# Optimization experiments

Measured on AMD Instinct MI355X. Metric: run time of the kernel, lower is better.

Reference implementation:

```python
import jax, jax.numpy as jnp
import numpy as np
from jax import lax

DT = 0.01
INPUT_SCALER = 20.0
BETA1 = 1.0


def setup_inputs() -> dict:
    key = jax.random.key(0)
    k1, k2, k3 = jax.random.split(key, 3)
    bs, T, d, nk = 8, 64, 32, 32
    X_r = jax.random.normal(k1, (bs, T, d, d, nk), dtype=jnp.float32)
    X_i = jax.random.normal(k2, (bs, T, d, d, nk), dtype=jnp.float32)
    # omegas ~ U(min_omega, max_omega) * 2*pi (Gaussian blur omitted: it only
    # smooths the fixed parameter initialization, not the forward math)
    min_omega, max_omega = 0.1, 1.0
    omegas = (jax.random.uniform(k3, (d, d, nk), dtype=jnp.float32)
              * (max_omega - min_omega) + min_omega) * (2 * 3.1415)
    return {"X_r": X_r, "X_i": X_i, "omegas": omegas}


def reference(X_r, X_i, omegas):
    bs, T, d1, d2, nk = X_r.shape
    # time-major for scan: [T, bs, d, d, nk]
    Xr_t = jnp.moveaxis(X_r, 1, 0)
    Xi_t = jnp.moveaxis(X_i, 1, 0)

    r0 = jnp.ones((bs, d1, d2, nk), dtype=X_r.dtype)
    phi0 = jnp.zeros((bs, d1, d2, nk), dtype=X_r.dtype)

    def step(carry, xs):
        r, phi = carry
        xr, xi = xs
        input_r = INPUT_SCALER * xr * jnp.cos(phi)
        input_phi = INPUT_SCALER * xi * jnp.sin(phi)
        r = r + ((1.0 - BETA1 * r * r) * r + input_r) * DT
        phi = phi + (omegas - input_phi) * DT
        return (r, phi), (r, phi)

    _, (r_arr, phi_arr) = lax.scan(step, (r0, phi0), (Xr_t, Xi_t))
    # back to batch-major: [bs, T, d, d, nk]
    r_arr = jnp.moveaxis(r_arr, 0, 1)
    phi_arr = jnp.moveaxis(phi_arr, 0, 1)
    return r_arr * jnp.cos(phi_arr), r_arr * jnp.sin(phi_arr)
```

## Files before the change

### kernel.cpp

```cpp
#include <hip/hip_runtime.h>


#define T_STEPS 64
#define CHV2    16384
#define BS      8
#define DEPTH   16

typedef float v2f __attribute__((ext_vector_type(2)));

__global__ __launch_bounds__(256)
void hopf_scan_kernel(const float* __restrict__ Xr,
                      const float* __restrict__ Xi,
                      const float* __restrict__ Om,
                      float* __restrict__ out)
{
    const float DT = 0.01f;
    const float SC = 20.0f;
    const float S1 = -1.6666667e-1f, S2 = 8.3333333e-3f,
                S3 = -1.9841270e-4f, S4 = 2.7557319e-6f;
    const float C1 = -0.5f, C2 = 4.1666667e-2f,
                C3 = -1.3888889e-3f, C4 = 2.4801587e-5f;

    const v2f* __restrict__ vXr = (const v2f*)Xr;
    const v2f* __restrict__ vXi = (const v2f*)Xi;
    const v2f* __restrict__ vOm = (const v2f*)Om;
    v2f* __restrict__ vout      = (v2f*)out;

    int tid = blockIdx.x * blockDim.x + threadIdx.x;
    int b   = tid >> 14;
    int cv  = tid & (CHV2 - 1);

    v2f om = vOm[cv];

    const size_t stride = CHV2;
    size_t base = (size_t)(b * T_STEPS) * stride + cv;
    const v2f* pxr = vXr + base;
    const v2f* pxi = vXi + base;
    v2f* po0 = vout + base;
    v2f* po1 = po0 + (size_t)BS * T_STEPS * stride;

    float r[2]  = {1.f, 1.f};
    float co[2] = {1.f, 1.f};
    float si[2] = {0.f, 0.f};

    v2f xr[DEPTH], xi[DEPTH];
    #pragma unroll
    for (int i = 0; i < DEPTH; ++i) {
        xr[i] = __builtin_nontemporal_load(pxr + (size_t)i * stride);
        xi[i] = __builtin_nontemporal_load(pxi + (size_t)i * stride);
    }

    #pragma unroll
    for (int t = 0; t < T_STEPS; ++t) {
        const int s = t & (DEPTH - 1);
        v2f axr = xr[s];
        v2f axi = xi[s];
        if (t + DEPTH < T_STEPS) {
            xr[s] = __builtin_nontemporal_load(pxr + (size_t)(t + DEPTH) * stride);
            xi[s] = __builtin_nontemporal_load(pxi + (size_t)(t + DEPTH) * stride);
        }

        v2f o0, o1;
        #pragma unroll
        for (int j = 0; j < 2; ++j) {
            float ir   = SC * axr[j] * co[j];
            float dphi = (om[j] - SC * axi[j] * si[j]) * DT;
            r[j] = r[j] + ((1.f - r[j] * r[j]) * r[j] + ir) * DT;

            float u  = dphi * dphi;
            float sp = fmaf(u, S4, S3);
            sp = fmaf(u, sp, S2);
            sp = fmaf(u, sp, S1);
            sp = fmaf(u, sp, 1.f);
            sp *= dphi;
            float cp = fmaf(u, C4, C3);
            cp = fmaf(u, cp, C2);
            cp = fmaf(u, cp, C1);
            cp = fmaf(u, cp, 1.f);

            float nco = fmaf(co[j], cp, -si[j] * sp);
            float nsi = fmaf(si[j], cp,  co[j] * sp);
            co[j] = nco; si[j] = nsi;

            o0[j] = r[j] * co[j];
            o1[j] = r[j] * si[j];
        }

        size_t off = (size_t)t * stride;
        po0[off] = o0;
        po1[off] = o1;
    }
}

extern "C" void kernel_launch(void* const* d_in, const int* in_sizes, int n_in,
                              void* d_out, int out_size, void* d_ws, size_t ws_size,
                              hipStream_t stream) {
    const float* Xr = (const float*)d_in[0];
    const float* Xi = (const float*)d_in[1];
    const float* Om = (const float*)d_in[2];
    float* out = (float*)d_out;

    dim3 block(256);
    dim3 grid(BS * CHV2 / 256);
    hopf_scan_kernel<<<grid, block, 0, stream>>>(Xr, Xi, Om, out);
}
```

Baseline: 225.7 us.

## Warp-specialize producer waves loading inputs into LDS ring via global_load_lds

Splits each 512-thread block into four producer waves that stream Xr/Xi time slices directly into a 4-slot LDS ring buffer with global_load_lds, and four consumer waves that read from LDS and run the recurrence. The two groups coordinate with barriers and explicit vmcnt waits. This replaces the per-thread register prefetch of 16 timesteps and is meant to cut register pressure and keep more loads in flight. The cost is barrier synchronization on every two timesteps, half of each block's waves doing no compute, and fragile hand-tuned waitcnt logic.

```diff
diff --git a/kernel.cpp b/kernel.cpp
--- a/kernel.cpp
+++ b/kernel.cpp
@@ -1,94 +1,138 @@
 #include <hip/hip_runtime.h>
+#include <stdint.h>
 
 
 #define T_STEPS 64
 #define CHV2    16384
 #define BS      8
-#define DEPTH   16
+#define CPB     256
+#define SLOTB   4096
 
 typedef float v2f __attribute__((ext_vector_type(2)));
+typedef __attribute__((address_space(3))) uint32_t as3_u32;
+typedef __attribute__((address_space(1))) uint32_t as1_u32;
 
-__global__ __launch_bounds__(256)
+__device__ __forceinline__ void gll16(const v2f* g, uint32_t lds_byte) {
+    __builtin_amdgcn_global_load_lds((const as1_u32*)g,
+                                     (as3_u32*)(uintptr_t)lds_byte,
+                                     16, 0, 2);
+}
+
+__global__ __launch_bounds__(512, 4)
 void hopf_scan_kernel(const float* __restrict__ Xr,
                       const float* __restrict__ Xi,
                       const float* __restrict__ Om,
                       float* __restrict__ out)
 {
-    const float DT = 0.01f;
-    const float SC = 20.0f;
+    __shared__ __align__(16) float lds[8 * SLOTB / 4];
+
+    const float DTS = 0.01f, SC = 20.0f;
     const float S1 = -1.6666667e-1f, S2 = 8.3333333e-3f,
                 S3 = -1.9841270e-4f, S4 = 2.7557319e-6f;
     const float C1 = -0.5f, C2 = 4.1666667e-2f,
                 C3 = -1.3888889e-3f, C4 = 2.4801587e-5f;
 
-    const v2f* __restrict__ vXr = (const v2f*)Xr;
-    const v2f* __restrict__ vXi = (const v2f*)Xi;
-    const v2f* __restrict__ vOm = (const v2f*)Om;
-    v2f* __restrict__ vout      = (v2f*)out;
+    const int wid  = threadIdx.x >> 6;
+    const int lane = threadIdx.x & 63;
+    const int blk  = blockIdx.x;
+    const int b    = blk >> 6;
+    const int cv0  = (blk & 63) * CPB;
+    const size_t TS = CHV2;
+    const size_t planebase = (size_t)(b * T_STEPS) * TS + cv0;
 
-    int tid = blockIdx.x * blockDim.x + threadIdx.x;
-    int b   = tid >> 14;
-    int cv  = tid & (CHV2 - 1);
+    const uint32_t ldsbase =
+        (uint32_t)(uintptr_t)(__attribute__((address_space(3))) float*)lds;
 
-    v2f om = vOm[cv];
+    if (wid < 4) {
+        const v2f* src = (wid < 2) ? (const v2f*)Xr : (const v2f*)Xi;
+        const v2f* gp  = src + planebase + 2 * ((wid & 1) * 64 + lane);
+        const uint32_t lboff = ldsbase + (uint32_t)((wid >> 1) * 2048 + (wid & 1) * 1024);
 
-    const size_t stride = CHV2;
-    size_t base = (size_t)(b * T_STEPS) * stride + cv;
-    const v2f* pxr = vXr + base;
-    const v2f* pxi = vXi + base;
-    v2f* po0 = vout + base;
-    v2f* po1 = po0 + (size_t)BS * T_STEPS * stride;
+        #pragma unroll
+        for (int t = 0; t < 6; ++t)
+            gll16(gp + (size_t)t * TS, lboff + (uint32_t)t * SLOTB);
+        asm volatile("s_waitcnt vmcnt(4)");
+        __builtin_amdgcn_s_barrier();
+        __builtin_amdgcn_sched_barrier(0);
 
-    float r[2]  = {1.f, 1.f};
-    float co[2] = {1.f, 1.f};
-    float si[2] = {0.f, 0.f};
+        const v2f* gq = gp + (size_t)6 * TS;
+        for (int w = 0; w < 32; ++w) {
+            if (w <= 28) {
+                uint32_t so = lboff + (uint32_t)(((w + 3) & 3) * 2) * SLOTB;
+                gll16(gq,      so);
+                gll16(gq + TS, so + SLOTB);
+                gq += 2 * TS;
+            }
+            if (w <= 28) {
+                asm volatile("s_waitcnt vmcnt(4)");
+            } else if (w < 31) {
+                asm volatile("s_waitcnt vmcnt(0)");
+            }
+            __builtin_amdgcn_s_barrier();
+            __builtin_amdgcn_sched_barrier(0);
+        }
+    } else {
+        const int ctid = threadIdx.x - 256;
+        v2f omv = ((const v2f*)Om)[cv0 + ctid];
+        float om[2] = {omv[0], omv[1]};
+        v2f* po0 = (v2f*)out + planebase + ctid;
+        v2f* po1 = po0 + (size_t)BS * T_STEPS * TS;
+        float r[2]  = {1.f, 1.f};
+        float co[2] = {1.f, 1.f};
+        float si[2] = {0.f, 0.f};
+        const uint32_t rbase = ldsbase + (uint32_t)ctid * 8;
 
-    v2f xr[DEPTH], xi[DEPTH];
-    #pragma unroll
-    for (int i = 0; i < DEPTH; ++i) {
-        xr[i] = __builtin_nontemporal_load(pxr + (size_t)i * stride);
-        xi[i] = __builtin_nontemporal_load(pxi + (size_t)i * stride);
-    }
+        __builtin_amdgcn_s_barrier();
+        __builtin_amdgcn_sched_barrier(0);
 
-    #pragma unroll
-    for (int t = 0; t < T_STEPS; ++t) {
-        const int s = t & (DEPTH - 1);
-        v2f axr = xr[s];
-        v2f axi = xi[s];
-        if (t + DEPTH < T_STEPS) {
-            xr[s] = __builtin_nontemporal_load(pxr + (size_t)(t + DEPTH) * stride);
-            xi[s] = __builtin_nontemporal_load(pxi + (size_t)(t + DEPTH) * stride);
+        auto stepf = [&](v2f axr, v2f axi, v2f& o0, v2f& o1) {
+            #pragma unroll
+            for (int j = 0; j < 2; ++j) {
+                float ir   = SC * axr[j] * co[j];
+                float dphi = (om[j] - SC * axi[j] * si[j]) * DTS;
+                r[j] = r[j] + ((1.f - r[j] * r[j]) * r[j] + ir) * DTS;
+                float u  = dphi * dphi;
+                float sp = fmaf(u, S4, S3);
+                sp = fmaf(u, sp, S2);
+                sp = fmaf(u, sp, S1);
+                sp = fmaf(u, sp, 1.f);
+                sp *= dphi;
+                float cp = fmaf(u, C4, C3);
+                cp = fmaf(u, cp, C2);
+                cp = fmaf(u, cp, C1);
+                cp = fmaf(u, cp, 1.f);
+                float nco = fmaf(co[j], cp, -si[j] * sp);
+                float nsi = fmaf(si[j], cp,  co[j] * sp);
+                co[j] = nco; si[j] = nsi;
+                o0[j] = r[j] * co[j];
+                o1[j] = r[j] * si[j];
+            }
+        };
+
+        for (int w = 0; w < 32; ++w) {
+            uint32_t ra0 = rbase + (uint32_t)((w & 3) * 2) * SLOTB;
+            uint32_t ra1 = ra0 + SLOTB;
+            v2f axr0, axi0, axr1, axi1;
+            asm volatile("ds_read_b64 %0, %4\n\t"
+                         "ds_read_b64 %1, %4 offset:2048\n\t"
+                         "ds_read_b64 %2, %5\n\t"
+                         "ds_read_b64 %3, %5 offset:2048\n\t"
+                         "s_waitcnt lgkmcnt(0)"
+                         : "=&v"(axr0), "=&v"(axi0), "=&v"(axr1), "=&v"(axi1)
+                         : "v"(ra0), "v"(ra1));
+            __builtin_amdgcn_sched_barrier(0);
+
+            v2f o0a, o1a, o0b, o1b;
+            stepf(axr0, axi0, o0a, o1a);
+            stepf(axr1, axi1, o0b, o1b);
+
+            po0[0]  = o0a;  po1[0]  = o1a;
+            po0[TS] = o0b;  po1[TS] = o1b;
+            po0 += 2 * TS;  po1 += 2 * TS;
+
+            __builtin_amdgcn_s_barrier();
+            __builtin_amdgcn_sched_barrier(0);
         }
-
-        v2f o0, o1;
-        #pragma unroll
-        for (int j = 0; j < 2; ++j) {
-            float ir   = SC * axr[j] * co[j];
-            float dphi = (om[j] - SC * axi[j] * si[j]) * DT;
-            r[j] = r[j] + ((1.f - r[j] * r[j]) * r[j] + ir) * DT;
-
-            float u  = dphi * dphi;
-            float sp = fmaf(u, S4, S3);
-            sp = fmaf(u, sp, S2);
-            sp = fmaf(u, sp, S1);
-            sp = fmaf(u, sp, 1.f);
-            sp *= dphi;
-            float cp = fmaf(u, C4, C3);
-            cp = fmaf(u, cp, C2);
-            cp = fmaf(u, cp, C1);
-            cp = fmaf(u, cp, 1.f);
-
-            float nco = fmaf(co[j], cp, -si[j] * sp);
-            float nsi = fmaf(si[j], cp,  co[j] * sp);
-            co[j] = nco; si[j] = nsi;
-
-            o0[j] = r[j] * co[j];
-            o1[j] = r[j] * si[j];
-        }
-
-        size_t off = (size_t)t * stride;
-        po0[off] = o0;
-        po1[off] = o1;
     }
 }
 
@@ -100,7 +144,7 @@
     const float* Om = (const float*)d_in[2];
     float* out = (float*)d_out;
 
-    dim3 block(256);
-    dim3 grid(BS * CHV2 / 256);
+    dim3 block(512);
+    dim3 grid(BS * CHV2 / CPB);
     hopf_scan_kernel<<<grid, block, 0, stream>>>(Xr, Xi, Om, out);
 }
```

New measurement: 230.1 us. About the same (+1.9%).
